# Kernel optimization log

Hardware: AMD Instinct MI355X
Metric: run time of the kernel (lower is better)

The kernel has to match this reference:

```python
import jax, jax.numpy as jnp
import numpy as np

NEG_SLOPE = 0.2

def setup_inputs() -> dict:
    key = jax.random.key(0)
    ks = jax.random.split(key, 10)
    N, E, F, H, C, NC, G = 50000, 800000, 256, 8, 32, 10, 128
    x = jax.random.normal(ks[0], (N, F), jnp.float32)
    W1 = jax.random.normal(ks[1], (F, H * C), jnp.float32) * (1.0 / np.sqrt(F))
    a_src1 = jax.random.normal(ks[2], (H, C), jnp.float32) * 0.1
    a_dst1 = jax.random.normal(ks[3], (H, C), jnp.float32) * 0.1
    b1 = jnp.zeros((H * C,), jnp.float32)
    W2 = jax.random.normal(ks[4], (H * C, NC), jnp.float32) * (1.0 / np.sqrt(H * C))
    a_src2 = jax.random.normal(ks[5], (1, NC), jnp.float32) * 0.1
    a_dst2 = jax.random.normal(ks[6], (1, NC), jnp.float32) * 0.1
    b2 = jnp.zeros((NC,), jnp.float32)
    edge_index = jax.random.randint(ks[7], (2, E), 0, N, jnp.int64)
    batch = jnp.sort(jax.random.randint(ks[8], (N,), 0, G, jnp.int64))
    return {"x": x, "W1": W1, "a_src1": a_src1, "a_dst1": a_dst1, "b1": b1,
            "W2": W2, "a_src2": a_src2, "a_dst2": a_dst2, "b2": b2,
            "edge_index": edge_index, "batch": batch}


def gat_conv(x, W, a_src, a_dst, b, src, dst, concat):
    # x: [N,F] -> h: [N,H,C]
    N = x.shape[0]
    H, C = a_src.shape
    h = (x @ W).reshape(N, H, C)
    alpha_s = jnp.einsum('nhc,hc->nh', h, a_src)  # [N,H]
    alpha_d = jnp.einsum('nhc,hc->nh', h, a_dst)  # [N,H]
    e = jax.nn.leaky_relu(alpha_s[src] + alpha_d[dst], NEG_SLOPE)  # [E,H]
    # segment softmax over edges sharing the same destination node
    m = jax.ops.segment_max(e, dst, num_segments=N)
    ex = jnp.exp(e - m[dst])
    s = jax.ops.segment_sum(ex, dst, num_segments=N)
    alpha = ex / s[dst]
    msg = h[src] * alpha[:, :, None]  # [E,H,C]
    out = jax.ops.segment_sum(msg, dst, num_segments=N)  # [N,H,C]
    out = out.reshape(N, H * C) if concat else out.mean(axis=1)
    return out + b


def reference(x, W1, a_src1, a_dst1, b1, W2, a_src2, a_dst2, b2, edge_index, batch):
    N = x.shape[0]
    G = 128
    loop = jnp.arange(N, dtype=edge_index.dtype)
    src = jnp.concatenate([edge_index[0], loop])  # add self loops (PyG default)
    dst = jnp.concatenate([edge_index[1], loop])
    # dropout layers are identity at inference (training=False)
    h = jax.nn.elu(gat_conv(x, W1, a_src1, a_dst1, b1, src, dst, concat=True))
    out = gat_conv(h, W2, a_src2, a_dst2, b2, src, dst, concat=False)  # [N,NC]
    # global mean pool over graphs
    sums = jax.ops.segment_sum(out, batch, num_segments=G)
    cnt = jax.ops.segment_sum(jnp.ones((N,), out.dtype), batch, num_segments=G)
    return sums / jnp.maximum(cnt, 1.0)[:, None]
```

## Files before the change

### kernel.cpp

```cpp
#include <hip/hip_runtime.h>
#include <hip/hip_bf16.h>
#include <math.h>

#define N_NODES 50000
#define N_EDGES 800000
#define E_TOT   (N_EDGES + N_NODES)
#define NCLS 10
#define NGRP 128

#define NBKT 196
#define EPB  1024
#define NB1  ((E_TOT + EPB - 1) / EPB)

typedef __attribute__((ext_vector_type(8))) short bf16x8;
typedef __attribute__((ext_vector_type(4))) float f32x4;
typedef __attribute__((ext_vector_type(2))) float f32x2;

static __device__ __forceinline__ ushort f2bf(float f) {
  union { float f; unsigned u; } v; v.f = f;
  unsigned r = v.u + 0x7fffu + ((v.u >> 16) & 1u);
  return (ushort)(r >> 16);
}
static __device__ __forceinline__ unsigned char enc8(float v) {
  int p = __builtin_amdgcn_cvt_pk_fp8_f32(v, v, 0, false);
  return (unsigned char)(p & 0xFF);
}
static __device__ __forceinline__ void fma4(float w, unsigned u, float* a) {
  f32x2 lo = __builtin_amdgcn_cvt_pk_f32_fp8(u, false);
  f32x2 hi = __builtin_amdgcn_cvt_pk_f32_fp8(u, true);
  a[0] += w * lo[0]; a[1] += w * lo[1]; a[2] += w * hi[0]; a[3] += w * hi[1];
}

#define CAST_BLOCKS 12500
#define W1T_BASE 12500
#define W2T_BASE 12564
#define WA_BASE  12565
#define PREP_BLOCKS 12566

__global__ __launch_bounds__(256) void prep_kernel(const float4* __restrict__ X4,
                                                   ushort4* __restrict__ Xb,
                                                   const float* __restrict__ W1,
                                                   ushort* __restrict__ W1t,
                                                   const float* __restrict__ W2,
                                                   ushort* __restrict__ W2tp,
                                                   const float* __restrict__ asrc1,
                                                   const float* __restrict__ adst1) {
  int b = blockIdx.x;
  int tid = threadIdx.x;
  if (b < CAST_BLOCKS) {
    int i = b * 256 + tid;
    float4 v = X4[i];
    ushort4 o;
    o.x = f2bf(v.x); o.y = f2bf(v.y); o.z = f2bf(v.z); o.w = f2bf(v.w);
    Xb[i] = o;
  } else if (b < W2T_BASE) {
    __shared__ float t[32][33];
    int bb = b - W1T_BASE;
    int k0 = (bb >> 3) * 32, n0 = (bb & 7) * 32;
    int tx = tid & 31, ty = tid >> 5;
    for (int r = 0; r < 32; r += 8)
      t[ty + r][tx] = W1[(k0 + ty + r) * 256 + n0 + tx];
    __syncthreads();
    for (int r = 0; r < 32; r += 8)
      W1t[(n0 + ty + r) * 256 + k0 + tx] = f2bf(t[tx][ty + r]);
  } else if (b == W2T_BASE) {
    int k = tid;
#pragma unroll
    for (int c = 0; c < 16; ++c)
      W2tp[c * 256 + k] = (c < NCLS) ? f2bf(W2[k * NCLS + c]) : (ushort)0;
  } else {
    int k = tid;
    const float* wrow = W1 + k * 256;
#pragma unroll
    for (int h = 0; h < 8; ++h) {
      float s = 0.f, d = 0.f;
#pragma unroll
      for (int c = 0; c < 32; ++c) {
        float w = wrow[h * 32 + c];
        s += w * asrc1[h * 32 + c];
        d += w * adst1[h * 32 + c];
      }
      W1t[(256 + h) * 256 + k] = f2bf(s);
      W1t[(264 + h) * 256 + k] = f2bf(d);
    }
  }
}

#define GEMM_BLOCKS ((N_NODES + 63) / 64)

__global__ __launch_bounds__(256) void gemm1_mfma(const ushort* __restrict__ Xb,
                                                  const ushort* __restrict__ W1t,
                                                  unsigned char* __restrict__ h1f8,
                                                  float* __restrict__ as1,
                                                  float* __restrict__ ad1) {
  __shared__ ushort As[32][64][8];
  int wid = threadIdx.x >> 6, lane = threadIdx.x & 63;
  int r = lane & 15, kg = lane >> 4;
  int m0 = blockIdx.x * 64;
  int n0 = wid * 64;
  bool extra = (wid == 3);

  {
    int mi = wid;
    int row = m0 + mi * 16 + r;
    if (row >= N_NODES) row = 0;
    const ushort* src = Xb + (size_t)row * 256 + kg * 8;
    bf16x8 v0 = *reinterpret_cast<const bf16x8*>(src);
    bf16x8 v1 = *reinterpret_cast<const bf16x8*>(src + 32);
    bf16x8 v2 = *reinterpret_cast<const bf16x8*>(src + 64);
    bf16x8 v3 = *reinterpret_cast<const bf16x8*>(src + 96);
    bf16x8 v4 = *reinterpret_cast<const bf16x8*>(src + 128);
    bf16x8 v5 = *reinterpret_cast<const bf16x8*>(src + 160);
    bf16x8 v6 = *reinterpret_cast<const bf16x8*>(src + 192);
    bf16x8 v7 = *reinterpret_cast<const bf16x8*>(src + 224);
    *reinterpret_cast<bf16x8*>(&As[mi * 8 + 0][lane][0]) = v0;
    *reinterpret_cast<bf16x8*>(&As[mi * 8 + 1][lane][0]) = v1;
    *reinterpret_cast<bf16x8*>(&As[mi * 8 + 2][lane][0]) = v2;
    *reinterpret_cast<bf16x8*>(&As[mi * 8 + 3][lane][0]) = v3;
    *reinterpret_cast<bf16x8*>(&As[mi * 8 + 4][lane][0]) = v4;
    *reinterpret_cast<bf16x8*>(&As[mi * 8 + 5][lane][0]) = v5;
    *reinterpret_cast<bf16x8*>(&As[mi * 8 + 6][lane][0]) = v6;
    *reinterpret_cast<bf16x8*>(&As[mi * 8 + 7][lane][0]) = v7;
  }
  __syncthreads();

  f32x4 acc[4][4];
  f32x4 accE[4];
#pragma unroll
  for (int mi = 0; mi < 4; ++mi) {
#pragma unroll
    for (int ni = 0; ni < 4; ++ni) acc[mi][ni] = 0;
    accE[mi] = 0;
  }

  const ushort* bptr[4];
#pragma unroll
  for (int ni = 0; ni < 4; ++ni)
    bptr[ni] = W1t + (size_t)(n0 + ni * 16 + r) * 256 + kg * 8;
  const ushort* bptrE = W1t + (size_t)(256 + r) * 256 + kg * 8;

#pragma unroll 2
  for (int ks = 0; ks < 8; ++ks) {
    int k0 = ks * 32;
    bf16x8 a[4], b[4], bE;
#pragma unroll
    for (int ni = 0; ni < 4; ++ni)
      b[ni] = *reinterpret_cast<const bf16x8*>(bptr[ni] + k0);
    if (extra) bE = *reinterpret_cast<const bf16x8*>(bptrE + k0);
#pragma unroll
    for (int mi = 0; mi < 4; ++mi)
      a[mi] = *reinterpret_cast<const bf16x8*>(&As[mi * 8 + ks][lane][0]);
#pragma unroll
    for (int mi = 0; mi < 4; ++mi) {
#pragma unroll
      for (int ni = 0; ni < 4; ++ni)
        acc[mi][ni] = __builtin_amdgcn_mfma_f32_16x16x32_bf16(a[mi], b[ni], acc[mi][ni], 0, 0, 0);
      if (extra)
        accE[mi] = __builtin_amdgcn_mfma_f32_16x16x32_bf16(a[mi], bE, accE[mi], 0, 0, 0);
    }
  }

#pragma unroll
  for (int mi = 0; mi < 4; ++mi) {
#pragma unroll
    for (int q = 0; q < 4; ++q) {
      int row = m0 + mi * 16 + kg * 4 + q;
      if (row < N_NODES) {
#pragma unroll
        for (int ni = 0; ni < 4; ++ni)
          h1f8[(size_t)row * 256 + n0 + ni * 16 + r] = enc8(acc[mi][ni][q]);
        if (extra) {
          float* dst = (r < 8) ? (as1 + row * 8 + r) : (ad1 + row * 8 + (r & 7));
          *dst = accE[mi][q];
        }
      }
    }
  }
}

__global__ __launch_bounds__(256) void k_hist(const int* __restrict__ ei,
                                              int* __restrict__ histg) {
  __shared__ int h[NBKT];
  int tid = threadIdx.x;
  for (int j = tid; j < NBKT; j += 256) h[j] = 0;
  __syncthreads();
  int base = blockIdx.x * EPB;
#pragma unroll
  for (int t = 0; t < 4; ++t) {
    int i = base + t * 256 + tid;
    if (i < E_TOT) {
      int d = (i < N_EDGES) ? ei[N_EDGES + i] : (i - N_EDGES);
      atomicAdd(&h[d >> 8], 1);
    }
  }
  __syncthreads();
  for (int j = tid; j < NBKT; j += 256) histg[j * NB1 + blockIdx.x] = h[j];
}

__global__ __launch_bounds__(256) void k_scan(int* __restrict__ histg,
                                              int* __restrict__ tot) {
  __shared__ int sh[256];
  int b = blockIdx.x, tid = threadIdx.x;
  int carry = 0;
  for (int c = 0; c < (NB1 + 255) / 256; ++c) {
    int j = c * 256 + tid;
    int v = (j < NB1) ? histg[b * NB1 + j] : 0;
    sh[tid] = v;
    __syncthreads();
    for (int d = 1; d < 256; d <<= 1) {
      int t = (tid >= d) ? sh[tid - d] : 0;
      __syncthreads();
      sh[tid] += t;
      __syncthreads();
    }
    if (j < NB1) histg[b * NB1 + j] = carry + sh[tid] - v;
    carry += sh[255];
    __syncthreads();
  }
  if (tid == 0) tot[b] = carry;
}

__global__ __launch_bounds__(256) void k_base(const int* __restrict__ tot,
                                              int* __restrict__ baseg) {
  __shared__ int sh[256];
  int tid = threadIdx.x;
  int v = (tid < NBKT) ? tot[tid] : 0;
  sh[tid] = v;
  __syncthreads();
  for (int d = 1; d < 256; d <<= 1) {
    int t = (tid >= d) ? sh[tid - d] : 0;
    __syncthreads();
    sh[tid] += t;
    __syncthreads();
  }
  if (tid < NBKT) baseg[tid] = sh[tid] - v;
  if (tid == 255) baseg[NBKT] = sh[255];
}

__global__ __launch_bounds__(256) void k_place(const int* __restrict__ ei,
                                               const int* __restrict__ histg,
                                               const int* __restrict__ baseg,
                                               unsigned int* __restrict__ cs) {
  __shared__ int h[NBKT];
  __shared__ int basec[NBKT];
  int tid = threadIdx.x;
  for (int j = tid; j < NBKT; j += 256) {
    h[j] = 0;
    basec[j] = baseg[j] + histg[j * NB1 + blockIdx.x];
  }
  __syncthreads();
  int base = blockIdx.x * EPB;
#pragma unroll
  for (int t = 0; t < 4; ++t) {
    int i = base + t * 256 + tid;
    if (i < E_TOT) {
      int s = (i < N_EDGES) ? ei[i] : (i - N_EDGES);
      int d = (i < N_EDGES) ? ei[N_EDGES + i] : (i - N_EDGES);
      int bk = d >> 8;
      int r = atomicAdd(&h[bk], 1);
      cs[basec[bk] + r] = ((unsigned)d << 16) | (unsigned)s;
    }
  }
}

__global__ __launch_bounds__(256) void k_fine(const unsigned int* __restrict__ cs,
                                              const int* __restrict__ baseg,
                                              int* __restrict__ csr,
                                              int* __restrict__ off) {
  __shared__ int cnt[256];
  __shared__ int sh[256];
  __shared__ int scn[256];
  __shared__ int cur[256];
  int b = blockIdx.x, tid = threadIdx.x;
  int lo = baseg[b], hi = baseg[b + 1];
  cnt[tid] = 0;
  cur[tid] = 0;
  __syncthreads();
  for (int i = lo + tid; i < hi; i += 256) atomicAdd(&cnt[(cs[i] >> 16) & 255], 1);
  __syncthreads();
  int v = cnt[tid];
  sh[tid] = v;
  __syncthreads();
  for (int d = 1; d < 256; d <<= 1) {
    int t = (tid >= d) ? sh[tid - d] : 0;
    __syncthreads();
    sh[tid] += t;
    __syncthreads();
  }
  scn[tid] = sh[tid] - v;
  int idx = b * 256 + tid;
  if (idx <= N_NODES) off[idx] = lo + scn[tid];
  __syncthreads();
  for (int i = lo + tid; i < hi; i += 256) {
    unsigned e = cs[i];
    int dl = (e >> 16) & 255;
    int r = atomicAdd(&cur[dl], 1);
    csr[lo + scn[dl] + r] = (int)(e & 0xFFFFu);
  }
}

__global__ __launch_bounds__(256) void agg1_kernel(const unsigned char* __restrict__ h1f8,
                                                   const float* __restrict__ as1,
                                                   const float* __restrict__ ad1,
                                                   const int* __restrict__ off,
                                                   const int* __restrict__ csr,
                                                   const float* __restrict__ b1,
                                                   ushort* __restrict__ h2b) {
  int n = (blockIdx.x * 256 + threadIdx.x) >> 6;
  int lane = threadIdx.x & 63;
  int p0 = off[n], p1 = off[n + 1];

  int sl = lane >> 4;
  int cl = lane & 15;
  int cb = cl * 16;
  int h = cl >> 1;
  float ad = ad1[n * 8 + h];

  float ssum = 0.f;
  float acc[16] = {};

  int p = p0 + sl;
  for (; p + 4 < p1; p += 8) {
    int sA = csr[p], sB = csr[p + 4];
    float eA = as1[sA * 8 + h] + ad;
    float eB = as1[sB * 8 + h] + ad;
    uint4 rA = *reinterpret_cast<const uint4*>(h1f8 + (size_t)sA * 256 + cb);
    uint4 rB = *reinterpret_cast<const uint4*>(h1f8 + (size_t)sB * 256 + cb);
    eA = eA > 0.f ? eA : 0.2f * eA;
    eB = eB > 0.f ? eB : 0.2f * eB;
    float wA = __expf(eA), wB = __expf(eB);
    ssum += wA + wB;
    fma4(wA, rA.x, acc);      fma4(wB, rB.x, acc);
    fma4(wA, rA.y, acc + 4);  fma4(wB, rB.y, acc + 4);
    fma4(wA, rA.z, acc + 8);  fma4(wB, rB.z, acc + 8);
    fma4(wA, rA.w, acc + 12); fma4(wB, rB.w, acc + 12);
  }
  for (; p < p1; p += 4) {
    int sA = csr[p];
    float eA = as1[sA * 8 + h] + ad;
    uint4 rA = *reinterpret_cast<const uint4*>(h1f8 + (size_t)sA * 256 + cb);
    eA = eA > 0.f ? eA : 0.2f * eA;
    float wA = __expf(eA);
    ssum += wA;
    fma4(wA, rA.x, acc);
    fma4(wA, rA.y, acc + 4);
    fma4(wA, rA.z, acc + 8);
    fma4(wA, rA.w, acc + 12);
  }

  ssum += __shfl_xor(ssum, 16); ssum += __shfl_xor(ssum, 32);
#pragma unroll
  for (int c = 0; c < 16; ++c) {
    acc[c] += __shfl_xor(acc[c], 16);
    acc[c] += __shfl_xor(acc[c], 32);
  }

  if (sl == 0) {
    float inv = 1.f / ssum;
    float o[16];
    float4 b0 = *reinterpret_cast<const float4*>(b1 + cb);
    float4 b1v = *reinterpret_cast<const float4*>(b1 + cb + 4);
    float4 b2v = *reinterpret_cast<const float4*>(b1 + cb + 8);
    float4 b3v = *reinterpret_cast<const float4*>(b1 + cb + 12);
    float bb[16] = {b0.x, b0.y, b0.z, b0.w, b1v.x, b1v.y, b1v.z, b1v.w,
                    b2v.x, b2v.y, b2v.z, b2v.w, b3v.x, b3v.y, b3v.z, b3v.w};
#pragma unroll
    for (int c = 0; c < 16; ++c) {
      float v = acc[c] * inv + bb[c];
      o[c] = v > 0.f ? v : __expf(v) - 1.f;
    }
    int4 o0, o1;
    o0.x = (int)(((unsigned)f2bf(o[1]) << 16) | f2bf(o[0]));
    o0.y = (int)(((unsigned)f2bf(o[3]) << 16) | f2bf(o[2]));
    o0.z = (int)(((unsigned)f2bf(o[5]) << 16) | f2bf(o[4]));
    o0.w = (int)(((unsigned)f2bf(o[7]) << 16) | f2bf(o[6]));
    o1.x = (int)(((unsigned)f2bf(o[9]) << 16) | f2bf(o[8]));
    o1.y = (int)(((unsigned)f2bf(o[11]) << 16) | f2bf(o[10]));
    o1.z = (int)(((unsigned)f2bf(o[13]) << 16) | f2bf(o[12]));
    o1.w = (int)(((unsigned)f2bf(o[15]) << 16) | f2bf(o[14]));
    *reinterpret_cast<int4*>(h2b + (size_t)n * 256 + cb) = o0;
    *reinterpret_cast<int4*>(h2b + (size_t)n * 256 + cb + 8) = o1;
  }
}

__global__ __launch_bounds__(256) void proj2_mfma(const ushort* __restrict__ h2b,
                                                  const ushort* __restrict__ W2tp,
                                                  const float* __restrict__ asrc2,
                                                  const float* __restrict__ adst2,
                                                  float* __restrict__ pj2p,
                                                  float* __restrict__ as2,
                                                  float* __restrict__ ad2) {
  int wid = threadIdx.x >> 6, lane = threadIdx.x & 63;
  int r = lane & 15, kg = lane >> 4;
  int rb = blockIdx.x * 64 + wid * 16;
  int row_a = rb + r;
  if (row_a >= N_NODES) row_a = 0;
  const ushort* ap = h2b + (size_t)row_a * 256 + kg * 8;
  const ushort* bp = W2tp + (size_t)r * 256 + kg * 8;
  f32x4 acc = 0;
#pragma unroll
  for (int k0 = 0; k0 < 256; k0 += 32)
    acc = __builtin_amdgcn_mfma_f32_16x16x32_bf16(
        *reinterpret_cast<const bf16x8*>(ap + k0),
        *reinterpret_cast<const bf16x8*>(bp + k0), acc, 0, 0, 0);

  float av = (r < NCLS) ? asrc2[r] : 0.f;
  float dv = (r < NCLS) ? adst2[r] : 0.f;
#pragma unroll
  for (int q = 0; q < 4; ++q) {
    int row = rb + kg * 4 + q;
    float v = acc[q];
    if (row < N_NODES) pj2p[row * 16 + r] = v;
    float s = v * av, d = v * dv;
    s += __shfl_xor(s, 1); s += __shfl_xor(s, 2); s += __shfl_xor(s, 4); s += __shfl_xor(s, 8);
    d += __shfl_xor(d, 1); d += __shfl_xor(d, 2); d += __shfl_xor(d, 4); d += __shfl_xor(d, 8);
    if (r == 0 && row < N_NODES) { as2[row] = s; ad2[row] = d; }
  }
}

__global__ __launch_bounds__(256) void agg2_kernel(const float* __restrict__ pj2p,
                                                   const float* __restrict__ as2,
                                                   const float* __restrict__ ad2,
                                                   const int* __restrict__ off,
                                                   const int* __restrict__ csr,
                                                   const float* __restrict__ b2,
                                                   float* __restrict__ out2p) {
  int n = (blockIdx.x * 256 + threadIdx.x) >> 6;
  int lane = threadIdx.x & 63;
  int p0 = off[n], p1 = off[n + 1];
  float ad = ad2[n];
  int es = lane >> 4, c = lane & 15;
  float ssum = 0.f, acc = 0.f;
  int p = p0 + es;
  for (; p + 12 < p1; p += 16) {
    int s0 = csr[p], s1 = csr[p + 4], s2 = csr[p + 8], s3 = csr[p + 12];
    float e0 = as2[s0] + ad, e1 = as2[s1] + ad, e2 = as2[s2] + ad, e3 = as2[s3] + ad;
    float v0 = pj2p[s0 * 16 + c], v1 = pj2p[s1 * 16 + c];
    float v2 = pj2p[s2 * 16 + c], v3 = pj2p[s3 * 16 + c];
    e0 = e0 > 0.f ? e0 : 0.2f * e0;
    e1 = e1 > 0.f ? e1 : 0.2f * e1;
    e2 = e2 > 0.f ? e2 : 0.2f * e2;
    e3 = e3 > 0.f ? e3 : 0.2f * e3;
    float w0 = __expf(e0), w1 = __expf(e1), w2 = __expf(e2), w3 = __expf(e3);
    ssum += (w0 + w1) + (w2 + w3);
    acc += (w0 * v0 + w1 * v1) + (w2 * v2 + w3 * v3);
  }
  for (; p < p1; p += 4) {
    int sA = csr[p];
    float eA = as2[sA] + ad;
    float vA = pj2p[sA * 16 + c];
    eA = eA > 0.f ? eA : 0.2f * eA;
    float wA = __expf(eA);
    ssum += wA;
    acc += wA * vA;
  }
  acc += __shfl_xor(acc, 16); acc += __shfl_xor(acc, 32);
  ssum += __shfl_xor(ssum, 16); ssum += __shfl_xor(ssum, 32);
  if (lane < 16) {
    float bc = (lane < NCLS) ? b2[lane] : 0.f;
    out2p[n * 16 + lane] = acc / ssum + bc;
  }
}

__global__ __launch_bounds__(256) void pool_kernel(const float* __restrict__ out2p,
                                                   const int* __restrict__ batch,
                                                   float* __restrict__ outp) {
  __shared__ float red[256];
  int g = blockIdx.x;
  int lo = 0, hi = N_NODES;
  while (lo < hi) { int mid = (lo + hi) >> 1; if (batch[mid] < g) lo = mid + 1; else hi = mid; }
  int start = lo;
  hi = N_NODES;
  while (lo < hi) { int mid = (lo + hi) >> 1; if (batch[mid] < g + 1) lo = mid + 1; else hi = mid; }
  int end = lo;
  int t = threadIdx.x;
  int c = t & 15, nsl = t >> 4;
  float loc = 0.f;
  for (int nn = start + nsl; nn < end; nn += 16) loc += out2p[nn * 16 + c];
  red[t] = loc;
  __syncthreads();
  for (int s = 128; s >= 16; s >>= 1) {
    if (t < s) red[t] += red[t + s];
    __syncthreads();
  }
  if (t < NCLS) {
    float denom = fmaxf((float)(end - start), 1.f);
    outp[g * NCLS + t] = red[t] / denom;
  }
}

extern "C" void kernel_launch(void* const* d_in, const int* in_sizes, int n_in,
                              void* d_out, int out_size, void* d_ws, size_t ws_size,
                              hipStream_t stream) {
  const float* x      = (const float*)d_in[0];
  const float* W1     = (const float*)d_in[1];
  const float* a_src1 = (const float*)d_in[2];
  const float* a_dst1 = (const float*)d_in[3];
  const float* b1     = (const float*)d_in[4];
  const float* W2     = (const float*)d_in[5];
  const float* a_src2 = (const float*)d_in[6];
  const float* a_dst2 = (const float*)d_in[7];
  const float* b2     = (const float*)d_in[8];
  const int*   ei     = (const int*)d_in[9];
  const int*   batch  = (const int*)d_in[10];

  char* ws = (char*)d_ws;
  size_t o = 0;
  auto alloc = [&](size_t bytes) {
    char* p = ws + o;
    o = (o + bytes + 255) & ~(size_t)255;
    return p;
  };
  ushort* xb   = (ushort*)alloc((size_t)N_NODES * 256 * 2);
  ushort* w1t  = (ushort*)alloc((size_t)272 * 256 * 2);
  ushort* w2tp = (ushort*)alloc((size_t)16 * 256 * 2);
  unsigned char* h1f8 = (unsigned char*)alloc((size_t)N_NODES * 256);
  ushort* h2b  = (ushort*)alloc((size_t)N_NODES * 256 * 2);
  float* as1   = (float*)alloc((size_t)N_NODES * 8 * 4);
  float* ad1   = (float*)alloc((size_t)N_NODES * 8 * 4);
  float* pj2p  = (float*)alloc((size_t)N_NODES * 16 * 4);
  float* as2   = (float*)alloc((size_t)N_NODES * 4);
  float* ad2   = (float*)alloc((size_t)N_NODES * 4);
  float* out2p = (float*)alloc((size_t)N_NODES * 16 * 4);
  int*   histg = (int*)alloc((size_t)NBKT * NB1 * 4);
  int*   tot   = (int*)alloc((size_t)NBKT * 4);
  int*   baseg = (int*)alloc((size_t)(NBKT + 1) * 4);
  unsigned int* cs = (unsigned int*)alloc((size_t)E_TOT * 4);
  int*   csr   = (int*)alloc((size_t)E_TOT * 4);
  int*   off   = (int*)alloc((size_t)(N_NODES + 1) * 4);

  prep_kernel<<<PREP_BLOCKS, 256, 0, stream>>>((const float4*)x, (ushort4*)xb,
                                               W1, w1t, W2, w2tp, a_src1, a_dst1);
  gemm1_mfma<<<GEMM_BLOCKS, 256, 0, stream>>>(xb, w1t, h1f8, as1, ad1);

  k_hist<<<NB1, 256, 0, stream>>>(ei, histg);
  k_scan<<<NBKT, 256, 0, stream>>>(histg, tot);
  k_base<<<1, 256, 0, stream>>>(tot, baseg);
  k_place<<<NB1, 256, 0, stream>>>(ei, histg, baseg, cs);
  k_fine<<<NBKT, 256, 0, stream>>>(cs, baseg, csr, off);

  agg1_kernel<<<N_NODES / 4, 256, 0, stream>>>(h1f8, as1, ad1, off, csr, b1, h2b);
  proj2_mfma<<<GEMM_BLOCKS, 256, 0, stream>>>(h2b, w2tp, a_src2, a_dst2,
                                              pj2p, as2, ad2);
  agg2_kernel<<<N_NODES / 4, 256, 0, stream>>>(pj2p, as2, ad2, off, csr, b2, out2p);
  pool_kernel<<<NGRP, 256, 0, stream>>>(out2p, batch, (float*)d_out);
}
```

Measured before the change: 269.8 us.

## Fuse histogram into prep kernel, pre-scale CSR indices, use packed FMA accumulation

Moves the edge-destination histogram into the prep kernel as extra blocks, removing one launch and letting it run alongside the cast work. The cast now uses a grid-stride loop with far fewer blocks. CSR entries store the source index shifted left by 8, so the aggregation kernels form byte and element offsets with shifts instead of multiplies. Layer-1 accumulation uses float2 vector ops that may map to packed FMA. The shifted index assumes node counts fit in 24 bits and changes the meaning of csr for every consumer.

```diff
diff --git a/kernel.cpp b/kernel.cpp
--- a/kernel.cpp
+++ b/kernel.cpp
@@ -25,17 +25,19 @@
   int p = __builtin_amdgcn_cvt_pk_fp8_f32(v, v, 0, false);
   return (unsigned char)(p & 0xFF);
 }
-static __device__ __forceinline__ void fma4(float w, unsigned u, float* a) {
-  f32x2 lo = __builtin_amdgcn_cvt_pk_f32_fp8(u, false);
-  f32x2 hi = __builtin_amdgcn_cvt_pk_f32_fp8(u, true);
-  a[0] += w * lo[0]; a[1] += w * lo[1]; a[2] += w * hi[0]; a[3] += w * hi[1];
-}
-
-#define CAST_BLOCKS 12500
-#define W1T_BASE 12500
-#define W2T_BASE 12564
-#define WA_BASE  12565
-#define PREP_BLOCKS 12566
+static __device__ __forceinline__ void fma4p(float w, unsigned u, f32x2* a) {
+  f32x2 w2; w2[0] = w; w2[1] = w;
+  a[0] += w2 * __builtin_amdgcn_cvt_pk_f32_fp8(u, false);
+  a[1] += w2 * __builtin_amdgcn_cvt_pk_f32_fp8(u, true);
+}
+
+#define CAST_BLOCKS 2048
+#define NX4 (N_NODES * 64)
+#define W1T_BASE CAST_BLOCKS
+#define W2T_BASE (W1T_BASE + 64)
+#define WA_BASE  (W2T_BASE + 1)
+#define HIST_BASE (WA_BASE + 1)
+#define PREP_BLOCKS (HIST_BASE + NB1)
 
 __global__ __launch_bounds__(256) void prep_kernel(const float4* __restrict__ X4,
                                                    ushort4* __restrict__ Xb,
@@ -44,15 +46,18 @@
                                                    const float* __restrict__ W2,
                                                    ushort* __restrict__ W2tp,
                                                    const float* __restrict__ asrc1,
-                                                   const float* __restrict__ adst1) {
+                                                   const float* __restrict__ adst1,
+                                                   const int* __restrict__ ei,
+                                                   int* __restrict__ histg) {
   int b = blockIdx.x;
   int tid = threadIdx.x;
   if (b < CAST_BLOCKS) {
-    int i = b * 256 + tid;
-    float4 v = X4[i];
-    ushort4 o;
-    o.x = f2bf(v.x); o.y = f2bf(v.y); o.z = f2bf(v.z); o.w = f2bf(v.w);
-    Xb[i] = o;
+    for (int i = b * 256 + tid; i < NX4; i += CAST_BLOCKS * 256) {
+      float4 v = X4[i];
+      ushort4 o;
+      o.x = f2bf(v.x); o.y = f2bf(v.y); o.z = f2bf(v.z); o.w = f2bf(v.w);
+      Xb[i] = o;
+    }
   } else if (b < W2T_BASE) {
     __shared__ float t[32][33];
     int bb = b - W1T_BASE;
@@ -68,7 +73,7 @@
 #pragma unroll
     for (int c = 0; c < 16; ++c)
       W2tp[c * 256 + k] = (c < NCLS) ? f2bf(W2[k * NCLS + c]) : (ushort)0;
-  } else {
+  } else if (b == WA_BASE) {
     int k = tid;
     const float* wrow = W1 + k * 256;
 #pragma unroll
@@ -83,6 +88,22 @@
       W1t[(256 + h) * 256 + k] = f2bf(s);
       W1t[(264 + h) * 256 + k] = f2bf(d);
     }
+  } else {
+    __shared__ int h[NBKT];
+    int bb = b - HIST_BASE;
+    for (int j = tid; j < NBKT; j += 256) h[j] = 0;
+    __syncthreads();
+    int base = bb * EPB;
+#pragma unroll
+    for (int t = 0; t < 4; ++t) {
+      int i = base + t * 256 + tid;
+      if (i < E_TOT) {
+        int d = (i < N_EDGES) ? ei[N_EDGES + i] : (i - N_EDGES);
+        atomicAdd(&h[d >> 8], 1);
+      }
+    }
+    __syncthreads();
+    for (int j = tid; j < NBKT; j += 256) histg[j * NB1 + bb] = h[j];
   }
 }
 
@@ -178,25 +199,6 @@
   }
 }
 
-__global__ __launch_bounds__(256) void k_hist(const int* __restrict__ ei,
-                                              int* __restrict__ histg) {
-  __shared__ int h[NBKT];
-  int tid = threadIdx.x;
-  for (int j = tid; j < NBKT; j += 256) h[j] = 0;
-  __syncthreads();
-  int base = blockIdx.x * EPB;
-#pragma unroll
-  for (int t = 0; t < 4; ++t) {
-    int i = base + t * 256 + tid;
-    if (i < E_TOT) {
-      int d = (i < N_EDGES) ? ei[N_EDGES + i] : (i - N_EDGES);
-      atomicAdd(&h[d >> 8], 1);
-    }
-  }
-  __syncthreads();
-  for (int j = tid; j < NBKT; j += 256) histg[j * NB1 + blockIdx.x] = h[j];
-}
-
 __global__ __launch_bounds__(256) void k_scan(int* __restrict__ histg,
                                               int* __restrict__ tot) {
   __shared__ int sh[256];
@@ -295,7 +297,7 @@
     unsigned e = cs[i];
     int dl = (e >> 16) & 255;
     int r = atomicAdd(&cur[dl], 1);
-    csr[lo + scn[dl] + r] = (int)(e & 0xFFFFu);
+    csr[lo + scn[dl] + r] = (int)((e & 0xFFFFu) << 8);
   }
 }
 
@@ -317,42 +319,46 @@
   float ad = ad1[n * 8 + h];
 
   float ssum = 0.f;
-  float acc[16] = {};
+  f32x2 acc2[8];
+#pragma unroll
+  for (int j = 0; j < 8; ++j) { acc2[j][0] = 0.f; acc2[j][1] = 0.f; }
 
   int p = p0 + sl;
   for (; p + 4 < p1; p += 8) {
-    int sA = csr[p], sB = csr[p + 4];
-    float eA = as1[sA * 8 + h] + ad;
-    float eB = as1[sB * 8 + h] + ad;
-    uint4 rA = *reinterpret_cast<const uint4*>(h1f8 + (size_t)sA * 256 + cb);
-    uint4 rB = *reinterpret_cast<const uint4*>(h1f8 + (size_t)sB * 256 + cb);
+    int vA = csr[p], vB = csr[p + 4];
+    float eA = as1[(vA >> 5) + h] + ad;
+    float eB = as1[(vB >> 5) + h] + ad;
+    uint4 rA = *reinterpret_cast<const uint4*>(h1f8 + vA + cb);
+    uint4 rB = *reinterpret_cast<const uint4*>(h1f8 + vB + cb);
     eA = eA > 0.f ? eA : 0.2f * eA;
     eB = eB > 0.f ? eB : 0.2f * eB;
     float wA = __expf(eA), wB = __expf(eB);
     ssum += wA + wB;
-    fma4(wA, rA.x, acc);      fma4(wB, rB.x, acc);
-    fma4(wA, rA.y, acc + 4);  fma4(wB, rB.y, acc + 4);
-    fma4(wA, rA.z, acc + 8);  fma4(wB, rB.z, acc + 8);
-    fma4(wA, rA.w, acc + 12); fma4(wB, rB.w, acc + 12);
+    fma4p(wA, rA.x, acc2 + 0); fma4p(wB, rB.x, acc2 + 0);
+    fma4p(wA, rA.y, acc2 + 2); fma4p(wB, rB.y, acc2 + 2);
+    fma4p(wA, rA.z, acc2 + 4); fma4p(wB, rB.z, acc2 + 4);
+    fma4p(wA, rA.w, acc2 + 6); fma4p(wB, rB.w, acc2 + 6);
   }
   for (; p < p1; p += 4) {
-    int sA = csr[p];
-    float eA = as1[sA * 8 + h] + ad;
-    uint4 rA = *reinterpret_cast<const uint4*>(h1f8 + (size_t)sA * 256 + cb);
+    int vA = csr[p];
+    float eA = as1[(vA >> 5) + h] + ad;
+    uint4 rA = *reinterpret_cast<const uint4*>(h1f8 + vA + cb);
     eA = eA > 0.f ? eA : 0.2f * eA;
     float wA = __expf(eA);
     ssum += wA;
-    fma4(wA, rA.x, acc);
-    fma4(wA, rA.y, acc + 4);
-    fma4(wA, rA.z, acc + 8);
-    fma4(wA, rA.w, acc + 12);
+    fma4p(wA, rA.x, acc2 + 0);
+    fma4p(wA, rA.y, acc2 + 2);
+    fma4p(wA, rA.z, acc2 + 4);
+    fma4p(wA, rA.w, acc2 + 6);
   }
 
   ssum += __shfl_xor(ssum, 16); ssum += __shfl_xor(ssum, 32);
 #pragma unroll
-  for (int c = 0; c < 16; ++c) {
-    acc[c] += __shfl_xor(acc[c], 16);
-    acc[c] += __shfl_xor(acc[c], 32);
+  for (int j = 0; j < 8; ++j) {
+    acc2[j][0] += __shfl_xor(acc2[j][0], 16);
+    acc2[j][0] += __shfl_xor(acc2[j][0], 32);
+    acc2[j][1] += __shfl_xor(acc2[j][1], 16);
+    acc2[j][1] += __shfl_xor(acc2[j][1], 32);
   }
 
   if (sl == 0) {
@@ -366,7 +372,7 @@
                     b2v.x, b2v.y, b2v.z, b2v.w, b3v.x, b3v.y, b3v.z, b3v.w};
 #pragma unroll
     for (int c = 0; c < 16; ++c) {
-      float v = acc[c] * inv + bb[c];
+      float v = acc2[c >> 1][c & 1] * inv + bb[c];
       o[c] = v > 0.f ? v : __expf(v) - 1.f;
     }
     int4 o0, o1;
@@ -433,26 +439,27 @@
   float ssum = 0.f, acc = 0.f;
   int p = p0 + es;
   for (; p + 12 < p1; p += 16) {
-    int s0 = csr[p], s1 = csr[p + 4], s2 = csr[p + 8], s3 = csr[p + 12];
-    float e0 = as2[s0] + ad, e1 = as2[s1] + ad, e2 = as2[s2] + ad, e3 = as2[s3] + ad;
-    float v0 = pj2p[s0 * 16 + c], v1 = pj2p[s1 * 16 + c];
-    float v2 = pj2p[s2 * 16 + c], v3 = pj2p[s3 * 16 + c];
+    int v0 = csr[p], v1 = csr[p + 4], v2 = csr[p + 8], v3 = csr[p + 12];
+    float e0 = as2[v0 >> 8] + ad, e1 = as2[v1 >> 8] + ad;
+    float e2 = as2[v2 >> 8] + ad, e3 = as2[v3 >> 8] + ad;
+    float q0 = pj2p[(v0 >> 4) + c], q1 = pj2p[(v1 >> 4) + c];
+    float q2 = pj2p[(v2 >> 4) + c], q3 = pj2p[(v3 >> 4) + c];
     e0 = e0 > 0.f ? e0 : 0.2f * e0;
     e1 = e1 > 0.f ? e1 : 0.2f * e1;
     e2 = e2 > 0.f ? e2 : 0.2f * e2;
     e3 = e3 > 0.f ? e3 : 0.2f * e3;
     float w0 = __expf(e0), w1 = __expf(e1), w2 = __expf(e2), w3 = __expf(e3);
     ssum += (w0 + w1) + (w2 + w3);
-    acc += (w0 * v0 + w1 * v1) + (w2 * v2 + w3 * v3);
+    acc += (w0 * q0 + w1 * q1) + (w2 * q2 + w3 * q3);
   }
   for (; p < p1; p += 4) {
-    int sA = csr[p];
-    float eA = as2[sA] + ad;
-    float vA = pj2p[sA * 16 + c];
+    int vA = csr[p];
+    float eA = as2[vA >> 8] + ad;
+    float qA = pj2p[(vA >> 4) + c];
     eA = eA > 0.f ? eA : 0.2f * eA;
     float wA = __expf(eA);
     ssum += wA;
-    acc += wA * vA;
+    acc += wA * qA;
   }
   acc += __shfl_xor(acc, 16); acc += __shfl_xor(acc, 32);
   ssum += __shfl_xor(ssum, 16); ssum += __shfl_xor(ssum, 32);
@@ -530,10 +537,10 @@
   int*   off   = (int*)alloc((size_t)(N_NODES + 1) * 4);
 
   prep_kernel<<<PREP_BLOCKS, 256, 0, stream>>>((const float4*)x, (ushort4*)xb,
-                                               W1, w1t, W2, w2tp, a_src1, a_dst1);
+                                               W1, w1t, W2, w2tp, a_src1, a_dst1,
+                                               ei, histg);
   gemm1_mfma<<<GEMM_BLOCKS, 256, 0, stream>>>(xb, w1t, h1f8, as1, ad1);
 
-  k_hist<<<NB1, 256, 0, stream>>>(ei, histg);
   k_scan<<<NBKT, 256, 0, stream>>>(histg, tot);
   k_base<<<1, 256, 0, stream>>>(tot, baseg);
   k_place<<<NB1, 256, 0, stream>>>(ei, histg, baseg, cs);
```

Measured after the change: 264.9 us. Within noise of the previous version (-1.8%).
